# Optimization experiments

Measured on AMD Instinct MI355X. Metric: run time of the kernel, lower is better.

## Reference

```python
import jax, jax.numpy as jnp
import numpy as np

TEMPERATURE = 0.1
BASE_TEMPERATURE = 0.07
N = 8192
D = 128


def setup_inputs() -> dict:
    key = jax.random.key(0)
    kf, kl = jax.random.split(key)
    feats = jax.random.normal(kf, (N, 1, D), dtype=jnp.float32)
    # contrastive embeddings are typically L2-normalized upstream
    feats = feats / jnp.linalg.norm(feats, axis=-1, keepdims=True)
    labels = jax.random.randint(kl, (N,), 0, 2, dtype=jnp.int32)
    return {"feats": feats, "labels": labels}


def reference(feats, labels):
    # feats: [anchor_num, n_view=1, D]; labels: [anchor_num] binary fg/bg
    anchor_num, n_view, d = feats.shape
    n = anchor_num * n_view  # n_view == 1 in this module
    contrast_feature = feats.reshape(n, d)

    lab = labels.reshape(-1, 1)
    pos_mask = (lab == lab.T).astype(feats.dtype)  # [N, N]
    neg_mask = 1.0 - pos_mask

    # [N, N] similarity logits
    logits = jnp.matmul(contrast_feature, contrast_feature.T) / TEMPERATURE
    logits_max = jax.lax.stop_gradient(jnp.max(logits, axis=1, keepdims=True))
    logits = logits - logits_max

    # mask out self-contrast on the diagonal (logits_mask in torch code)
    idx = jnp.arange(n)
    pos_mask = pos_mask.at[idx, idx].set(0.0)

    exp_logits = jnp.exp(logits)
    neg_logits = jnp.sum(exp_logits * neg_mask, axis=1, keepdims=True)  # [N,1]
    log_prob = logits - jnp.log(exp_logits + neg_logits)

    mean_log_prob_pos = jnp.sum(pos_mask * log_prob, axis=1) / jnp.sum(pos_mask, axis=1)
    loss = -(TEMPERATURE / BASE_TEMPERATURE) * mean_log_prob_pos
    return jnp.mean(loss)
```

## Files before the change

kernel.cpp:

```cpp
#include <hip/hip_runtime.h>
#include <hip/hip_bf16.h>

#define NN 8192
#define DD 128

typedef short bf16x8 __attribute__((ext_vector_type(8)));
typedef float f32x4 __attribute__((ext_vector_type(4)));

#define CSCALE  3.7982829f
#define SLSCALE 2.6327684f

#define LABF_OFF (NN * DD * 2)
#define G_OFF    (LABF_OFF + NN * 4)
#define CNT_OFF  (G_OFF + 1024)
#define CTR2_OFF (G_OFF + 1028)
#define ACC_OFF  (G_OFF + 1032)
#define CTR_OFF  (G_OFF + 1152)
#define EG_OFF   (G_OFF + 1280)
#define ELG_OFF  (EG_OFF + NN * 4)

#define BROWS 256
#define BCOLS 512
#define TCOLS 32
#define ITERS (BCOLS / TCOLS)

__device__ __forceinline__ unsigned short f2bf(float x) {
    unsigned u = __float_as_uint(x);
    u = (u + 0x7FFFu + ((u >> 16) & 1u)) >> 16;
    return (unsigned short)u;
}

__global__ __launch_bounds__(256) void prep_kernel(const float* __restrict__ F,
        const int* __restrict__ labels, unsigned short* __restrict__ F16,
        float* __restrict__ labf, float* __restrict__ G,
        int* __restrict__ cnt1, float* __restrict__ Eg, float* __restrict__ Elg) {
    __shared__ float sG[256];
    __shared__ int scnt;
    const int tid = threadIdx.x;
    sG[tid] = 0.f;
    if (tid == 0) scnt = 0;
    __syncthreads();
    const int wave = tid >> 6, lane = tid & 63;
    const int half = lane >> 5, l32 = lane & 31;
    const int rb = blockIdx.x * 32;
    if (tid < 32) { Eg[rb + tid] = 0.f; Elg[rb + tid] = 0.f; }
    int mycnt = 0;
    float g1a[4] = {0.f, 0.f, 0.f, 0.f}, gta[4] = {0.f, 0.f, 0.f, 0.f};
    #pragma unroll
    for (int it = 0; it < 4; ++it) {
        const int row = rb + it * 8 + wave * 2 + half;
        const int lab = labels[row];
        const float lf = (float)lab;
        const float4 f = *reinterpret_cast<const float4*>(F + row * DD + l32 * 4);
        ushort4 u;
        u.x = f2bf(CSCALE * f.x); u.y = f2bf(CSCALE * f.y);
        u.z = f2bf(CSCALE * f.z); u.w = f2bf(CSCALE * f.w);
        *reinterpret_cast<ushort4*>(F16 + row * DD + l32 * 4) = u;
        g1a[0] = fmaf(lf, f.x, g1a[0]); gta[0] += f.x;
        g1a[1] = fmaf(lf, f.y, g1a[1]); gta[1] += f.y;
        g1a[2] = fmaf(lf, f.z, g1a[2]); gta[2] += f.z;
        g1a[3] = fmaf(lf, f.w, g1a[3]); gta[3] += f.w;
        if (l32 == 0) {
            labf[row] = lf;
            mycnt += lab;
        }
    }
    #pragma unroll
    for (int j = 0; j < 4; ++j) {
        atomicAdd(&sG[l32 * 4 + j], g1a[j]);
        atomicAdd(&sG[128 + l32 * 4 + j], gta[j]);
    }
    if (l32 == 0 && mycnt) atomicAdd(&scnt, mycnt);
    __syncthreads();
    atomicAdd(&G[tid], sG[tid]);
    if (tid == 0) atomicAdd(cnt1, scnt);
}

__global__ __launch_bounds__(512, 4) void loss_kernel(
        const unsigned short* __restrict__ F16, const float* __restrict__ labf,
        const int* __restrict__ labels, const float* __restrict__ G,
        const int* __restrict__ cnt1, float* __restrict__ Eg,
        float* __restrict__ Elg, int* __restrict__ ctr, int* __restrict__ ctr2,
        float* __restrict__ acc, float* __restrict__ out) {
    __shared__ unsigned short Bt[2][TCOLS * DD];
    __shared__ float Lab[BCOLS];
    __shared__ int sLast;
    __shared__ float wsum[8];
    const int tid  = threadIdx.x;
    const int wave = tid >> 6, lane = tid & 63;
    const int quad = lane >> 4, l16 = lane & 15;
    const int rg = blockIdx.x & 31;
    const int rb = rg * BROWS;
    const int cb = (blockIdx.x >> 5) * BCOLS;

    Lab[tid] = labf[cb + tid];

    const int rw = rb + wave * 32;
    bf16x8 a[2][4];
    #pragma unroll
    for (int m = 0; m < 2; m++)
        #pragma unroll
        for (int kb = 0; kb < 4; kb++)
            a[m][kb] = *reinterpret_cast<const bf16x8*>(
                F16 + (rw + m * 16 + l16) * DD + kb * 32 + quad * 8);

    const int scol = tid >> 4;
    const int sc   = tid & 15;
    const unsigned short* sbase = F16 + (cb + scol) * DD + sc * 8;
    const int sdst = sc * (TCOLS * 8) + (((scol ^ sc) & 31) * 8);

    *reinterpret_cast<bf16x8*>(&Bt[0][sdst]) =
        *reinterpret_cast<const bf16x8*>(sbase);

    float accE[2][4] = {}, accEl[2][4] = {};
    __syncthreads();

    for (int it = 0; it < ITERS; ++it) {
        const int cur = it & 1;
        const int itn = (it + 1) & (ITERS - 1);
        const bf16x8 vn = *reinterpret_cast<const bf16x8*>(sbase + itn * TCOLS * DD);

        #pragma unroll
        for (int g = 0; g < 2; ++g) {
            bf16x8 bfr[4];
            #pragma unroll
            for (int kb = 0; kb < 4; kb++) {
                const int cr = kb * 4 + quad;
                const int col = g * 16 + l16;
                bfr[kb] = *reinterpret_cast<const bf16x8*>(
                    &Bt[cur][cr * (TCOLS * 8) + (((col ^ cr) & 31) * 8)]);
            }
            f32x4 d0 = {0.f, 0.f, 0.f, 0.f}, d1 = {0.f, 0.f, 0.f, 0.f};
            #pragma unroll
            for (int kb = 0; kb < 4; kb++) {
                d0 = __builtin_amdgcn_mfma_f32_16x16x32_bf16(a[0][kb], bfr[kb], d0, 0, 0, 0);
                d1 = __builtin_amdgcn_mfma_f32_16x16x32_bf16(a[1][kb], bfr[kb], d1, 0, 0, 0);
            }
            const float lc = Lab[it * TCOLS + g * 16 + l16];
            #pragma unroll
            for (int r = 0; r < 4; r++) {
                const float e0 = exp2f(d0[r]);
                accE[0][r] += e0; accEl[0][r] = fmaf(lc, e0, accEl[0][r]);
                const float e1 = exp2f(d1[r]);
                accE[1][r] += e1; accEl[1][r] = fmaf(lc, e1, accEl[1][r]);
            }
        }

        *reinterpret_cast<bf16x8*>(&Bt[cur ^ 1][sdst]) = vn;
        __syncthreads();
    }

    #pragma unroll
    for (int m = 0; m < 2; m++) {
        #pragma unroll
        for (int r = 0; r < 4; r++) {
            float e = accE[m][r], el = accEl[m][r];
            #pragma unroll
            for (int off = 1; off < 16; off <<= 1) {
                e  += __shfl_xor(e,  off);
                el += __shfl_xor(el, off);
            }
            if (l16 == 0) {
                const int row = rw + m * 16 + quad * 4 + r;
                atomicAdd(&Eg[row], e);
                atomicAdd(&Elg[row], el);
            }
        }
    }

    __syncthreads();
    if (tid == 0) sLast = (atomicAdd(&ctr[rg], 1) == 15);
    __syncthreads();
    if (!sLast) return;

    if (tid < 256) Lab[tid] = G[tid];
    __syncthreads();

    float li = 0.f;
    if (tid < 256) {
        const int row = rb + tid;
        const int lr  = labels[row];
        const float E  = atomicAdd(&Eg[row], 0.f);
        const float El = atomicAdd(&Elg[row], 0.f);
        float dot = 0.f;
        const unsigned short* fp = F16 + row * DD;
        #pragma unroll
        for (int k = 0; k < DD; k += 8) {
            const bf16x8 fv = *reinterpret_cast<const bf16x8*>(fp + k);
            #pragma unroll
            for (int j = 0; j < 8; j++) {
                const float fj = __uint_as_float(((unsigned)(unsigned short)fv[j]) << 16);
                const float g1 = Lab[k + j];
                const float gl = lr ? g1 : (Lab[128 + k + j] - g1);
                dot = fmaf(fj, gl, dot);
            }
        }
        const float Epos = lr ? El : (E - El);
        const float Si   = E - Epos;
        const int   c1   = *cnt1;
        const float cntp1 = (float)(lr ? c1 : (NN - c1));
        const float cntm  = cntp1 - 1.f;
        const float sum_l   = SLSCALE * dot;
        const float sum_log = cntp1 * __logf(Si) + Epos / Si;
        li = -(10.f / 7.f) * (sum_l - sum_log) / cntm;
    }
    #pragma unroll
    for (int off = 1; off < 64; off <<= 1) li += __shfl_xor(li, off);
    if ((tid & 63) == 0) wsum[tid >> 6] = li;
    __syncthreads();
    if (tid == 0) {
        const float s = ((wsum[0] + wsum[1]) + (wsum[2] + wsum[3]))
                      + ((wsum[4] + wsum[5]) + (wsum[6] + wsum[7]));
        atomicAdd(acc, s * (1.0f / NN));
        __threadfence();
        if (atomicAdd(ctr2, 1) == 31) out[0] = atomicAdd(acc, 0.f);
    }
}

extern "C" void kernel_launch(void* const* d_in, const int* in_sizes, int n_in,
                              void* d_out, int out_size, void* d_ws, size_t ws_size,
                              hipStream_t stream) {
    const float* F      = (const float*)d_in[0];
    const int*   labels = (const int*)d_in[1];
    float*       out    = (float*)d_out;
    char*        ws     = (char*)d_ws;
    unsigned short* F16 = (unsigned short*)ws;
    float*       labf   = (float*)(ws + LABF_OFF);
    float*       G      = (float*)(ws + G_OFF);
    int*         cnt1   = (int*)(ws + CNT_OFF);
    int*         ctr2   = (int*)(ws + CTR2_OFF);
    float*       acc    = (float*)(ws + ACC_OFF);
    int*         ctr    = (int*)(ws + CTR_OFF);
    float*       Eg     = (float*)(ws + EG_OFF);
    float*       Elg    = (float*)(ws + ELG_OFF);

    hipMemsetAsync(ws + G_OFF, 0, 1280, stream);

    prep_kernel<<<NN / 32, 256, 0, stream>>>(F, labels, F16, labf, G, cnt1, Eg, Elg);
    loss_kernel<<<512, 512, 0, stream>>>(F16, labf, labels, G, cnt1,
                                         Eg, Elg, ctr, ctr2, acc, out);
}
```

Measured before the change: 100.6 us.

## Accumulate logit sums in main loop, drop memset and global feature-sum reduction

Removes the hipMemsetAsync and the prep kernel's label-weighted feature-sum reduction. The positive-logit sum is now accumulated directly in the MFMA loop (plain and label-weighted), and label counts are accumulated per row group inside the loss kernel. Counters are zeroed in the prep kernel instead. This saves one launch and shared and global atomics in prep and removes the per-row dot in the tail. In exchange the hot loop gains extra adds and FMAs per element, more registers, and extra atomics.

After: 118.1 us. 17.3% more time.

```diff
diff --git a/kernel.cpp b/kernel.cpp
--- a/kernel.cpp
+++ b/kernel.cpp
@@ -8,16 +8,16 @@
 typedef float f32x4 __attribute__((ext_vector_type(4)));
 
 #define CSCALE  3.7982829f
-#define SLSCALE 2.6327684f
-
-#define LABF_OFF (NN * DD * 2)
-#define G_OFF    (LABF_OFF + NN * 4)
-#define CNT_OFF  (G_OFF + 1024)
-#define CTR2_OFF (G_OFF + 1028)
-#define ACC_OFF  (G_OFF + 1032)
-#define CTR_OFF  (G_OFF + 1152)
-#define EG_OFF   (G_OFF + 1280)
+#define LN2     0.69314718056f
+
+#define CTR_OFF  (NN * DD * 2)
+#define CTRC_OFF (CTR_OFF + 128)
+#define CTR2_OFF (CTRC_OFF + 128)
+#define ACC_OFF  (CTR2_OFF + 4)
+#define EG_OFF   (CTRC_OFF + 256)
 #define ELG_OFF  (EG_OFF + NN * 4)
+#define SG_OFF   (ELG_OFF + NN * 4)
+#define SLG_OFF  (SG_OFF + NN * 4)
 
 #define BROWS 256
 #define BCOLS 512
@@ -31,57 +31,41 @@
 }
 
 __global__ __launch_bounds__(256) void prep_kernel(const float* __restrict__ F,
-        const int* __restrict__ labels, unsigned short* __restrict__ F16,
-        float* __restrict__ labf, float* __restrict__ G,
-        int* __restrict__ cnt1, float* __restrict__ Eg, float* __restrict__ Elg) {
-    __shared__ float sG[256];
-    __shared__ int scnt;
+        unsigned short* __restrict__ F16,
+        int* __restrict__ ctr, float* __restrict__ ctrC,
+        int* __restrict__ ctr2, float* __restrict__ acc,
+        float* __restrict__ Eg, float* __restrict__ Elg,
+        float* __restrict__ Sg, float* __restrict__ Slg) {
     const int tid = threadIdx.x;
-    sG[tid] = 0.f;
-    if (tid == 0) scnt = 0;
-    __syncthreads();
     const int wave = tid >> 6, lane = tid & 63;
     const int half = lane >> 5, l32 = lane & 31;
     const int rb = blockIdx.x * 32;
-    if (tid < 32) { Eg[rb + tid] = 0.f; Elg[rb + tid] = 0.f; }
-    int mycnt = 0;
-    float g1a[4] = {0.f, 0.f, 0.f, 0.f}, gta[4] = {0.f, 0.f, 0.f, 0.f};
+    if (tid < 32) {
+        Eg[rb + tid] = 0.f; Elg[rb + tid] = 0.f;
+        Sg[rb + tid] = 0.f; Slg[rb + tid] = 0.f;
+    }
+    if (blockIdx.x == 0) {
+        if (tid < 32) { ctr[tid] = 0; ctrC[tid] = 0.f; }
+        if (tid == 32) *ctr2 = 0;
+        if (tid == 33) *acc = 0.f;
+    }
     #pragma unroll
     for (int it = 0; it < 4; ++it) {
         const int row = rb + it * 8 + wave * 2 + half;
-        const int lab = labels[row];
-        const float lf = (float)lab;
         const float4 f = *reinterpret_cast<const float4*>(F + row * DD + l32 * 4);
         ushort4 u;
         u.x = f2bf(CSCALE * f.x); u.y = f2bf(CSCALE * f.y);
         u.z = f2bf(CSCALE * f.z); u.w = f2bf(CSCALE * f.w);
         *reinterpret_cast<ushort4*>(F16 + row * DD + l32 * 4) = u;
-        g1a[0] = fmaf(lf, f.x, g1a[0]); gta[0] += f.x;
-        g1a[1] = fmaf(lf, f.y, g1a[1]); gta[1] += f.y;
-        g1a[2] = fmaf(lf, f.z, g1a[2]); gta[2] += f.z;
-        g1a[3] = fmaf(lf, f.w, g1a[3]); gta[3] += f.w;
-        if (l32 == 0) {
-            labf[row] = lf;
-            mycnt += lab;
-        }
-    }
-    #pragma unroll
-    for (int j = 0; j < 4; ++j) {
-        atomicAdd(&sG[l32 * 4 + j], g1a[j]);
-        atomicAdd(&sG[128 + l32 * 4 + j], gta[j]);
-    }
-    if (l32 == 0 && mycnt) atomicAdd(&scnt, mycnt);
-    __syncthreads();
-    atomicAdd(&G[tid], sG[tid]);
-    if (tid == 0) atomicAdd(cnt1, scnt);
+    }
 }
 
 __global__ __launch_bounds__(512, 4) void loss_kernel(
-        const unsigned short* __restrict__ F16, const float* __restrict__ labf,
-        const int* __restrict__ labels, const float* __restrict__ G,
-        const int* __restrict__ cnt1, float* __restrict__ Eg,
-        float* __restrict__ Elg, int* __restrict__ ctr, int* __restrict__ ctr2,
-        float* __restrict__ acc, float* __restrict__ out) {
+        const unsigned short* __restrict__ F16, const int* __restrict__ labels,
+        float* __restrict__ ctrC, int* __restrict__ ctr, int* __restrict__ ctr2,
+        float* __restrict__ acc, float* __restrict__ Eg,
+        float* __restrict__ Elg, float* __restrict__ Sg,
+        float* __restrict__ Slg, float* __restrict__ out) {
     __shared__ unsigned short Bt[2][TCOLS * DD];
     __shared__ float Lab[BCOLS];
     __shared__ int sLast;
@@ -93,7 +77,7 @@
     const int rb = rg * BROWS;
     const int cb = (blockIdx.x >> 5) * BCOLS;
 
-    Lab[tid] = labf[cb + tid];
+    Lab[tid] = (float)labels[cb + tid];
 
     const int rw = rb + wave * 32;
     bf16x8 a[2][4];
@@ -113,7 +97,15 @@
         *reinterpret_cast<const bf16x8*>(sbase);
 
     float accE[2][4] = {}, accEl[2][4] = {};
-    __syncthreads();
+    float accS[2][4] = {}, accSl[2][4] = {};
+    __syncthreads();
+
+    {
+        float cc = Lab[wave * 64 + lane];
+        #pragma unroll
+        for (int off = 1; off < 64; off <<= 1) cc += __shfl_xor(cc, off);
+        if (lane == 0) atomicAdd(&ctrC[rg], cc);
+    }
 
     for (int it = 0; it < ITERS; ++it) {
         const int cur = it & 1;
@@ -141,8 +133,10 @@
             for (int r = 0; r < 4; r++) {
                 const float e0 = exp2f(d0[r]);
                 accE[0][r] += e0; accEl[0][r] = fmaf(lc, e0, accEl[0][r]);
+                accS[0][r] += d0[r]; accSl[0][r] = fmaf(lc, d0[r], accSl[0][r]);
                 const float e1 = exp2f(d1[r]);
                 accE[1][r] += e1; accEl[1][r] = fmaf(lc, e1, accEl[1][r]);
+                accS[1][r] += d1[r]; accSl[1][r] = fmaf(lc, d1[r], accSl[1][r]);
             }
         }
 
@@ -155,15 +149,20 @@
         #pragma unroll
         for (int r = 0; r < 4; r++) {
             float e = accE[m][r], el = accEl[m][r];
+            float s = accS[m][r], sl = accSl[m][r];
             #pragma unroll
             for (int off = 1; off < 16; off <<= 1) {
                 e  += __shfl_xor(e,  off);
                 el += __shfl_xor(el, off);
+                s  += __shfl_xor(s,  off);
+                sl += __shfl_xor(sl, off);
             }
             if (l16 == 0) {
                 const int row = rw + m * 16 + quad * 4 + r;
                 atomicAdd(&Eg[row], e);
                 atomicAdd(&Elg[row], el);
+                atomicAdd(&Sg[row], s);
+                atomicAdd(&Slg[row], sl);
             }
         }
     }
@@ -172,9 +171,6 @@
     if (tid == 0) sLast = (atomicAdd(&ctr[rg], 1) == 15);
     __syncthreads();
     if (!sLast) return;
-
-    if (tid < 256) Lab[tid] = G[tid];
-    __syncthreads();
 
     float li = 0.f;
     if (tid < 256) {
@@ -182,25 +178,14 @@
         const int lr  = labels[row];
         const float E  = atomicAdd(&Eg[row], 0.f);
         const float El = atomicAdd(&Elg[row], 0.f);
-        float dot = 0.f;
-        const unsigned short* fp = F16 + row * DD;
-        #pragma unroll
-        for (int k = 0; k < DD; k += 8) {
-            const bf16x8 fv = *reinterpret_cast<const bf16x8*>(fp + k);
-            #pragma unroll
-            for (int j = 0; j < 8; j++) {
-                const float fj = __uint_as_float(((unsigned)(unsigned short)fv[j]) << 16);
-                const float g1 = Lab[k + j];
-                const float gl = lr ? g1 : (Lab[128 + k + j] - g1);
-                dot = fmaf(fj, gl, dot);
-            }
-        }
+        const float S  = atomicAdd(&Sg[row], 0.f);
+        const float Sl = atomicAdd(&Slg[row], 0.f);
+        const float c1f = atomicAdd(&ctrC[rg], 0.f);
         const float Epos = lr ? El : (E - El);
         const float Si   = E - Epos;
-        const int   c1   = *cnt1;
-        const float cntp1 = (float)(lr ? c1 : (NN - c1));
+        const float cntp1 = lr ? c1f : ((float)NN - c1f);
         const float cntm  = cntp1 - 1.f;
-        const float sum_l   = SLSCALE * dot;
+        const float sum_l   = (lr ? Sl : (S - Sl)) * LN2;
         const float sum_log = cntp1 * __logf(Si) + Epos / Si;
         li = -(10.f / 7.f) * (sum_l - sum_log) / cntm;
     }
@@ -225,18 +210,17 @@
     float*       out    = (float*)d_out;
     char*        ws     = (char*)d_ws;
     unsigned short* F16 = (unsigned short*)ws;
-    float*       labf   = (float*)(ws + LABF_OFF);
-    float*       G      = (float*)(ws + G_OFF);
-    int*         cnt1   = (int*)(ws + CNT_OFF);
+    int*         ctr    = (int*)(ws + CTR_OFF);
+    float*       ctrC   = (float*)(ws + CTRC_OFF);
     int*         ctr2   = (int*)(ws + CTR2_OFF);
     float*       acc    = (float*)(ws + ACC_OFF);
-    int*         ctr    = (int*)(ws + CTR_OFF);
     float*       Eg     = (float*)(ws + EG_OFF);
     float*       Elg    = (float*)(ws + ELG_OFF);
-
-    hipMemsetAsync(ws + G_OFF, 0, 1280, stream);
-
-    prep_kernel<<<NN / 32, 256, 0, stream>>>(F, labels, F16, labf, G, cnt1, Eg, Elg);
-    loss_kernel<<<512, 512, 0, stream>>>(F16, labf, labels, G, cnt1,
-                                         Eg, Elg, ctr, ctr2, acc, out);
-}
+    float*       Sg     = (float*)(ws + SG_OFF);
+    float*       Slg    = (float*)(ws + SLG_OFF);
+
+    prep_kernel<<<NN / 32, 256, 0, stream>>>(F, F16, ctr, ctrC, ctr2, acc,
+                                             Eg, Elg, Sg, Slg);
+    loss_kernel<<<512, 512, 0, stream>>>(F16, labels, ctrC, ctr, ctr2, acc,
+                                         Eg, Elg, Sg, Slg, out);
+}
```
